# Kernel tuning notes

Measured on AMD Instinct MI355X. Metric: run time of the kernel, lower is better.

Reference implementation:

```python
import jax, jax.numpy as jnp
import numpy as np

B, T, V = 8, 2048, 1024


def setup_inputs() -> dict:
    key = jax.random.key(0)
    k1, k2, k3, k4, k5 = jax.random.split(key, 5)
    idx = jax.random.randint(k1, (B, T), 0, V)
    # nn.Embedding(length, 1) weight, std=0.02
    v = 0.02 * jax.random.normal(k2, (T, 1), dtype=jnp.float32)
    # nn.Linear(V, V, bias=False) weights (torch layout: out x in), std=0.02
    Wk = 0.02 * jax.random.normal(k3, (V, V), dtype=jnp.float32)
    Wq = 0.02 * jax.random.normal(k4, (V, V), dtype=jnp.float32)
    Wv = 0.02 * jax.random.normal(k5, (V, V), dtype=jnp.float32)
    return {"idx": idx, "v": v, "Wk": Wk, "Wq": Wq, "Wv": Wv}


def reference(idx, v, Wk, Wq, Wv):
    Tn = v.shape[0]
    Vn = Wk.shape[0]
    # one-hot token embedding [B, T, V]
    e = jax.nn.one_hot(idx, Vn, dtype=jnp.float32)
    # relative positions, clipped at 0; pos_embd[i, j] = v[i-j] for i >= j else 0
    pos = jnp.arange(Tn)
    rel = jnp.clip(pos[:, None] - pos[None, :], 0)
    pos_embd = jnp.tril(v[rel, 0])  # [T, T]
    # layer_one = pos_embd @ e  -> [B, T, V]
    layer_one = jnp.einsum('ts,bsv->btv', pos_embd, e)
    K = layer_one @ Wk.T           # Linear: x @ W^T
    Q = e @ Wq.T
    attention = jnp.einsum('btv,bsv->bts', Q, K)  # [B, T, T]
    causal = jnp.tril(jnp.ones((Tn, Tn), dtype=bool))
    masked_attention = jnp.where(causal, attention, 0.0)
    output = jnp.einsum('bts,bsv->btv', masked_attention, e @ Wv.T)
    logits = output + 0.001
    return logits
```

## Files before the change

kernel.cpp:

```cpp
#include <hip/hip_runtime.h>
#include <stdint.h>

#define T_DIM 2048
#define V_DIM 1024
#define B_DIM 8
#define NT 16

typedef unsigned int u32;
typedef unsigned short u16;
typedef __attribute__((ext_vector_type(8))) short s16x8;
typedef __attribute__((ext_vector_type(4))) float f32x4;

__device__ __forceinline__ u16 f2bf(float x) {
  u32 u = __builtin_bit_cast(u32, x);
  u = u + 0x7FFFu + ((u >> 16) & 1u);
  return (u16)(u >> 16);
}

#define GLD16(gp, lp) __builtin_amdgcn_global_load_lds( \
    (const __attribute__((address_space(1))) u32*)(gp), \
    (__attribute__((address_space(3))) u32*)(lp), 16, 0, 0)

template<int MODE, bool F32OUT>
__global__ void __launch_bounds__(256, 2)
gemm_bt(const u16* __restrict__ A, int lda, long long batchA,
        const u16* __restrict__ Bt, int ldb, long long batchB,
        void* __restrict__ Cv, int ldc, long long batchC,
        int K, float bias)
{
  int bn, bm, bz;
  if (MODE == 0) {
    bn = blockIdx.x; bm = blockIdx.y; bz = blockIdx.z;
  } else if (MODE == 1) {
    int lam = blockIdx.x;
    int tau = lam >> 3; bz = lam & 7;
    int b = NT - 1, off = 0;
    while (tau >= off + (NT - b)) { off += NT - b; b--; }
    bn = b; bm = b + (tau - off);
  } else {
    int lam = blockIdx.x;
    bm = (NT - 1) - (lam >> 6);
    bn = (lam >> 3) & 7;
    bz = lam & 7;
  }
  const u16* Ab = A + (long long)bz * batchA;
  const u16* Bb = Bt + (long long)bz * batchB;
  int m0 = bm * 128, n0 = bn * 128;
  int kmax = K;
  if (MODE == 1) { int kl = (bn + 1) * 128; kmax = kl < K ? kl : K; }
  if (MODE == 2) { int kl = (bm + 1) * 128; kmax = kl < K ? kl : K; }

  __shared__ u16 As[128 * 64];
  __shared__ u16 Bs[128 * 64];

  int tid = threadIdx.x;
  int lane = tid & 63;
  int wid = tid >> 6;
  int wm = wid >> 1, wn = wid & 1;

  f32x4 acc[4][4] = {};

  int r0 = tid >> 3;
  int gcol = (((tid & 7) - r0) & 7) * 8;
  const u16* ga = Ab + (long long)(m0 + r0) * lda + gcol;
  const u16* gb = Bb + (long long)(n0 + r0) * ldb + gcol;
  u16* la = As + tid * 8;
  u16* lb = Bs + tid * 8;
  long long lda32 = (long long)32 * lda;
  long long ldb32 = (long long)32 * ldb;

  int rm = lane & 15;
  int q = lane >> 4;

  for (int k0 = 0; k0 < kmax; k0 += 64) {
#pragma unroll
    for (int i = 0; i < 4; i++)
      GLD16(ga + k0 + i * lda32, la + i * 2048);
#pragma unroll
    for (int i = 0; i < 4; i++)
      GLD16(gb + k0 + i * ldb32, lb + i * 2048);
    __syncthreads();
#pragma unroll
    for (int ks = 0; ks < 2; ks++) {
      s16x8 af[4], bfv[4];
#pragma unroll
      for (int mi = 0; mi < 4; mi++) {
        int row = wm * 64 + mi * 16 + rm;
        int p = ((ks * 4 + q) + row) & 7;
        af[mi] = *(const s16x8*)&As[row * 64 + p * 8];
      }
#pragma unroll
      for (int ni = 0; ni < 4; ni++) {
        int row = wn * 64 + ni * 16 + rm;
        int p = ((ks * 4 + q) + row) & 7;
        bfv[ni] = *(const s16x8*)&Bs[row * 64 + p * 8];
      }
#pragma unroll
      for (int mi = 0; mi < 4; mi++)
#pragma unroll
        for (int ni = 0; ni < 4; ni++)
          acc[mi][ni] = __builtin_amdgcn_mfma_f32_16x16x32_bf16(
              af[mi], bfv[ni], acc[mi][ni], 0, 0, 0);
    }
    __syncthreads();
  }

  int col = lane & 15;
  int rq = (lane >> 4) * 4;
#pragma unroll
  for (int mi = 0; mi < 4; mi++) {
#pragma unroll
    for (int ni = 0; ni < 4; ni++) {
      int lr = wm * 64 + mi * 16 + rq;
      int lc = wn * 64 + ni * 16 + col;
#pragma unroll
      for (int rr = 0; rr < 4; rr++) {
        float val = acc[mi][ni][rr];
        if (MODE == 1 && (n0 + lc) > (m0 + lr + rr)) val = 0.f;
        long long off = (long long)(m0 + lr + rr) * ldc + (n0 + lc);
        if (F32OUT) {
          float* C = (float*)Cv + (long long)bz * batchC;
          C[off] = val + bias;
        } else {
          u16* C = (u16*)Cv + (long long)bz * batchC;
          C[off] = f2bf(val);
        }
      }
    }
  }
}

#define LDSB 24576
#define FENCE() asm volatile("" ::: "memory")

template<int MODE>
__global__ void __launch_bounds__(512, 2)
gemm8(const u16* __restrict__ Ag, int lda, long long batchA,
      const u16* __restrict__ Btg, int ldb, long long batchB,
      void* __restrict__ Cv, int ldc, long long batchC,
      float bias, int lnb)
{
  int lam = blockIdx.x;
  int bz = lam & ((1 << lnb) - 1);
  int tau = lam >> lnb;
  int m, n;
  if (MODE == 1) {
    int nn = 7, off = 0;
    while (tau >= off + (16 - 2 * nn)) { off += 16 - 2 * nn; nn--; }
    n = nn; m = 2 * nn + (tau - off);
  } else {
    m = 15 - (tau >> 2);
    n = tau & 3;
  }
  const int m0 = m * 128, n0 = n * 256;
  const int nk = (MODE == 1) ? (n + 1) * 4 : (m + 1) * 2;

  const u16* __restrict__ Ab = Ag + (long long)bz * batchA;
  const u16* __restrict__ Bb = Btg + (long long)bz * batchB;

  __shared__ u16 lds[3 * LDSB];

  const int tid = threadIdx.x;
  const int lane = tid & 63;
  const int wid = tid >> 6;
  const int wm = wid >> 2, wn = wid & 3;

  const u16* ga[2]; int la_[2];
#pragma unroll
  for (int i = 0; i < 2; i++) {
    int f = i * 512 + tid, r = f >> 3, c = ((f & 7) - r) & 7;
    ga[i] = Ab + (long long)(m0 + r) * lda + c * 8;
    la_[i] = f * 8;
  }
  const u16* gb[4]; int lb_[4];
#pragma unroll
  for (int i = 0; i < 4; i++) {
    int f = i * 512 + tid, r = f >> 3, c = ((f & 7) - r) & 7;
    gb[i] = Bb + (long long)(n0 + r) * ldb + c * 8;
    lb_[i] = 8192 + f * 8;
  }

  const int rm = lane & 15, q = lane >> 4;
  int aoff[4][2], boff[4][2];
#pragma unroll
  for (int mi = 0; mi < 4; mi++)
#pragma unroll
    for (int ks = 0; ks < 2; ks++) {
      int row = wm * 64 + mi * 16 + rm;
      aoff[mi][ks] = row * 64 + (((ks * 4 + q) + row) & 7) * 8;
    }
#pragma unroll
  for (int ni = 0; ni < 4; ni++)
#pragma unroll
    for (int ks = 0; ks < 2; ks++) {
      int row = wn * 64 + ni * 16 + rm;
      boff[ni][ks] = 8192 + row * 64 + (((ks * 4 + q) + row) & 7) * 8;
    }

  f32x4 acc[4][4] = {};

#pragma unroll
  for (int i = 0; i < 2; i++) GLD16(ga[i], &lds[la_[i]]);
#pragma unroll
  for (int i = 0; i < 4; i++) GLD16(gb[i], &lds[lb_[i]]);
#pragma unroll
  for (int i = 0; i < 2; i++) GLD16(ga[i] + 64, &lds[LDSB + la_[i]]);
#pragma unroll
  for (int i = 0; i < 4; i++) GLD16(gb[i] + 64, &lds[LDSB + lb_[i]]);

  int cb = 0;
  for (int kt = 0; kt < nk; ++kt) {
    if (kt + 1 < nk) asm volatile("s_waitcnt vmcnt(6)" ::: "memory");
    else             asm volatile("s_waitcnt vmcnt(0)" ::: "memory");
    __builtin_amdgcn_s_barrier();
    FENCE();

    const u16* Abuf = &lds[cb];
    int pb = cb + 2 * LDSB; if (pb >= 3 * LDSB) pb -= 3 * LDSB;
    const bool pf = (kt + 2) < nk;
    const int pk = (kt + 2) * 64;

    s16x8 af[4][2], bf0[2][2];
#pragma unroll
    for (int mi = 0; mi < 4; mi++)
#pragma unroll
      for (int ks = 0; ks < 2; ks++)
        af[mi][ks] = *(const s16x8*)&Abuf[aoff[mi][ks]];
#pragma unroll
    for (int ni = 0; ni < 2; ni++)
#pragma unroll
      for (int ks = 0; ks < 2; ks++)
        bf0[ni][ks] = *(const s16x8*)&Abuf[boff[ni][ks]];
    if (pf) {
      GLD16(ga[0] + pk, &lds[pb + la_[0]]);
      GLD16(ga[1] + pk, &lds[pb + la_[1]]);
      GLD16(gb[0] + pk, &lds[pb + lb_[0]]);
    }
    __builtin_amdgcn_s_barrier();
    FENCE();
    __builtin_amdgcn_s_setprio(1);
#pragma unroll
    for (int ks = 0; ks < 2; ks++)
#pragma unroll
      for (int mi = 0; mi < 4; mi++)
#pragma unroll
        for (int ni = 0; ni < 2; ni++)
          acc[mi][ni] = __builtin_amdgcn_mfma_f32_16x16x32_bf16(
              af[mi][ks], bf0[ni][ks], acc[mi][ni], 0, 0, 0);
    __builtin_amdgcn_s_setprio(0);
    __builtin_amdgcn_s_barrier();
    FENCE();

    s16x8 bf1[2][2];
#pragma unroll
    for (int ni = 0; ni < 2; ni++)
#pragma unroll
      for (int ks = 0; ks < 2; ks++)
        bf1[ni][ks] = *(const s16x8*)&Abuf[boff[ni + 2][ks]];
    if (pf) {
      GLD16(gb[1] + pk, &lds[pb + lb_[1]]);
      GLD16(gb[2] + pk, &lds[pb + lb_[2]]);
      GLD16(gb[3] + pk, &lds[pb + lb_[3]]);
    }
    __builtin_amdgcn_s_barrier();
    FENCE();
    __builtin_amdgcn_s_setprio(1);
#pragma unroll
    for (int ks = 0; ks < 2; ks++)
#pragma unroll
      for (int mi = 0; mi < 4; mi++)
#pragma unroll
        for (int ni = 0; ni < 2; ni++)
          acc[mi][ni + 2] = __builtin_amdgcn_mfma_f32_16x16x32_bf16(
              af[mi][ks], bf1[ni][ks], acc[mi][ni + 2], 0, 0, 0);
    __builtin_amdgcn_s_setprio(0);
    cb += LDSB; if (cb >= 3 * LDSB) cb = 0;
  }

  const int col = lane & 15, rq = (lane >> 4) * 4;
  if (MODE == 2) {
    float* C = (float*)Cv + (long long)bz * batchC;
#pragma unroll
    for (int mi = 0; mi < 4; mi++) {
      int lr = m0 + wm * 64 + mi * 16 + rq;
#pragma unroll
      for (int ni = 0; ni < 4; ni++) {
        int lc = n0 + wn * 64 + ni * 16 + col;
#pragma unroll
        for (int rr = 0; rr < 4; rr++)
          C[(long long)(lr + rr) * ldc + lc] = acc[mi][ni][rr] + bias;
      }
    }
  } else {
    u16* C = (u16*)Cv + (long long)bz * batchC;
#pragma unroll
    for (int mi = 0; mi < 4; mi++) {
      int lr = m0 + wm * 64 + mi * 16 + rq;
#pragma unroll
      for (int ni = 0; ni < 4; ni++) {
        int lc = n0 + wn * 64 + ni * 16 + col;
#pragma unroll
        for (int rr = 0; rr < 4; rr++) {
          float val = acc[mi][ni][rr];
          if (lc > lr + rr) val = 0.f;
          C[(long long)(lr + rr) * ldc + lc] = f2bf(val);
        }
      }
    }
  }
}

__global__ void prep_weights(const float* __restrict__ Wq, u16* __restrict__ WqT,
                             const float* __restrict__ Wk, u16* __restrict__ WkT,
                             const float* __restrict__ Wv, u16* __restrict__ Wvb)
{
  int z = blockIdx.z;
  if (z == 2) {
    int bx = blockIdx.y * 32 + blockIdx.x;
    int i = bx * 1024 + threadIdx.y * 32 + threadIdx.x;
#pragma unroll
    for (int k = 0; k < 4; k++) Wvb[i + k * 256] = f2bf(Wv[i + k * 256]);
    return;
  }
  const float* src = z ? Wk : Wq;
  u16* dst = z ? WkT : WqT;
  __shared__ float tile[32][33];
  int x0 = blockIdx.x * 32, y0 = blockIdx.y * 32;
  int tx = threadIdx.x, ty = threadIdx.y;
#pragma unroll
  for (int k = 0; k < 4; k++)
    tile[ty + k * 8][tx] = src[(long long)(y0 + ty + k * 8) * V_DIM + x0 + tx];
  __syncthreads();
#pragma unroll
  for (int k = 0; k < 4; k++)
    dst[(long long)(x0 + ty + k * 8) * V_DIM + y0 + tx] = f2bf(tile[tx][ty + k * 8]);
}

__global__ void build_p(const float* __restrict__ v, u16* __restrict__ P)
{
  int gid = blockIdx.x * 256 + threadIdx.x;
  int e0 = gid * 8;
  int s = e0 >> 11, u0 = e0 & 2047;
  s16x8 o;
#pragma unroll
  for (int k = 0; k < 8; k++) {
    int u = u0 + k;
    o[k] = (short)((u <= s) ? f2bf(v[s - u]) : (u16)0);
  }
  *(s16x8*)&P[e0] = o;
}

__global__ void __launch_bounds__(256)
gather_gy(const int* __restrict__ idx, const u16* __restrict__ Mb,
          const u16* __restrict__ Wvb, u16* __restrict__ G,
          u16* __restrict__ Yt, int b0)
{
  int bx = blockIdx.x, z = blockIdx.y;
  const int* idxrow = idx + (long long)(b0 + z) * T_DIM;
  __shared__ u16 Row[V_DIM];
  int tid = threadIdx.x;
  const u32* src;
  u16* dst;
  if (bx < T_DIM) {
    src = (const u32*)(Mb + (long long)idxrow[bx] * V_DIM);
    dst = G + ((long long)z * T_DIM + bx) * T_DIM;
  } else {
    src = (const u32*)(Wvb + (long long)(bx - T_DIM) * V_DIM);
    dst = Yt + ((long long)z * V_DIM + (bx - T_DIM)) * T_DIM;
  }
  u32* dstl = (u32*)Row;
  dstl[tid] = src[tid];
  dstl[tid + 256] = src[tid + 256];
  __syncthreads();
  int s0 = tid * 8;
  int4 i0 = *(const int4*)&idxrow[s0];
  int4 i1 = *(const int4*)&idxrow[s0 + 4];
  s16x8 o;
  o[0] = (short)Row[i0.x]; o[1] = (short)Row[i0.y];
  o[2] = (short)Row[i0.z]; o[3] = (short)Row[i0.w];
  o[4] = (short)Row[i1.x]; o[5] = (short)Row[i1.y];
  o[6] = (short)Row[i1.z]; o[7] = (short)Row[i1.w];
  *(s16x8*)&dst[s0] = o;
}

extern "C" void kernel_launch(void* const* d_in, const int* in_sizes, int n_in,
                              void* d_out, int out_size, void* d_ws, size_t ws_size,
                              hipStream_t stream)
{
  const int*   idx = (const int*)d_in[0];
  const float* v   = (const float*)d_in[1];
  const float* Wk  = (const float*)d_in[2];
  const float* Wq  = (const float*)d_in[3];
  const float* Wv  = (const float*)d_in[4];
  float* out = (float*)d_out;

  char* p = (char*)d_ws;
  const size_t SZ_VV = (size_t)V_DIM * V_DIM * 2;
  const size_t SZ_TT = (size_t)T_DIM * T_DIM * 2;
  const size_t SZ_VT = (size_t)V_DIM * T_DIM * 2;
  u16* WqT = (u16*)p; p += SZ_VV;
  u16* WkT = (u16*)p; p += SZ_VV;
  u16* Wvb = (u16*)p; p += SZ_VV;
  u16* Mb  = (u16*)p; p += SZ_VV;
  u16* P   = (u16*)p; p += SZ_TT;
  size_t used = (size_t)(p - (char*)d_ws);
  size_t per = 2 * SZ_TT + SZ_VT;
  int nb = 8;
  while (nb > 1 && used + (size_t)nb * per > ws_size) nb >>= 1;
  u16* G    = (u16*)p; p += (size_t)nb * SZ_TT;
  u16* Abuf = (u16*)p; p += (size_t)nb * SZ_TT;
  u16* Yt   = (u16*)p;
  int lnb = (nb == 8) ? 3 : (nb == 4) ? 2 : (nb == 2) ? 1 : 0;

  prep_weights<<<dim3(32, 32, 3), dim3(32, 8), 0, stream>>>(Wq, WqT, Wk, WkT, Wv, Wvb);
  build_p<<<2048, 256, 0, stream>>>(v, P);
  gemm_bt<0, false><<<dim3(V_DIM / 128, V_DIM / 128, 1), 256, 0, stream>>>(
      WqT, V_DIM, 0, WkT, V_DIM, 0, Mb, V_DIM, 0, V_DIM, 0.f);

  for (int b0 = 0; b0 < B_DIM; b0 += nb) {
    gather_gy<<<dim3(T_DIM + V_DIM, nb), 256, 0, stream>>>(idx, Mb, Wvb, G, Yt, b0);
    gemm8<1><<<dim3(72 * nb), 512, 0, stream>>>(
        G, T_DIM, (long long)T_DIM * T_DIM, P, T_DIM, 0,
        Abuf, T_DIM, (long long)T_DIM * T_DIM, 0.f, lnb);
    gemm8<2><<<dim3(64 * nb), 512, 0, stream>>>(
        Abuf, T_DIM, (long long)T_DIM * T_DIM, Yt, T_DIM, (long long)V_DIM * T_DIM,
        out + (long long)b0 * T_DIM * V_DIM, V_DIM, (long long)T_DIM * V_DIM,
        0.001f, lnb);
  }
}
```

Before: 203.9 us.

## Enlarge gemm8 tiles to 256x256 with double-buffered LDS and four-phase pipeline

The causal/triangular GEMM kernels move from 128x256 output tiles with a triple-buffered LDS ring to 256x256 tiles with two LDS buffers. Each wave now owns an 8x4 grid of MFMA accumulators, and the K-step is split into four MFMA phases with global-to-LDS prefetches interleaved between them. The goal is to raise arithmetic intensity and cut global and LDS traffic per FLOP. In exchange, accumulator register pressure doubles, the grid halves to fewer workgroups, and triangular work is handled at coarser granularity. The unused triangular modes of gemm_bt are also removed.

```diff
diff --git a/kernel.cpp b/kernel.cpp
--- a/kernel.cpp
+++ b/kernel.cpp
@@ -28,27 +28,11 @@
         void* __restrict__ Cv, int ldc, long long batchC,
         int K, float bias)
 {
-  int bn, bm, bz;
-  if (MODE == 0) {
-    bn = blockIdx.x; bm = blockIdx.y; bz = blockIdx.z;
-  } else if (MODE == 1) {
-    int lam = blockIdx.x;
-    int tau = lam >> 3; bz = lam & 7;
-    int b = NT - 1, off = 0;
-    while (tau >= off + (NT - b)) { off += NT - b; b--; }
-    bn = b; bm = b + (tau - off);
-  } else {
-    int lam = blockIdx.x;
-    bm = (NT - 1) - (lam >> 6);
-    bn = (lam >> 3) & 7;
-    bz = lam & 7;
-  }
+  int bn = blockIdx.x, bm = blockIdx.y, bz = blockIdx.z;
   const u16* Ab = A + (long long)bz * batchA;
   const u16* Bb = Bt + (long long)bz * batchB;
   int m0 = bm * 128, n0 = bn * 128;
   int kmax = K;
-  if (MODE == 1) { int kl = (bn + 1) * 128; kmax = kl < K ? kl : K; }
-  if (MODE == 2) { int kl = (bm + 1) * 128; kmax = kl < K ? kl : K; }
 
   __shared__ u16 As[128 * 64];
   __shared__ u16 Bs[128 * 64];
@@ -116,7 +100,6 @@
 #pragma unroll
       for (int rr = 0; rr < 4; rr++) {
         float val = acc[mi][ni][rr];
-        if (MODE == 1 && (n0 + lc) > (m0 + lr + rr)) val = 0.f;
         long long off = (long long)(m0 + lr + rr) * ldc + (n0 + lc);
         if (F32OUT) {
           float* C = (float*)Cv + (long long)bz * batchC;
@@ -130,7 +113,7 @@
   }
 }
 
-#define LDSB 24576
+#define LDSE 32768
 #define FENCE() asm volatile("" ::: "memory")
 
 template<int MODE>
@@ -146,98 +129,79 @@
   int m, n;
   if (MODE == 1) {
     int nn = 7, off = 0;
-    while (tau >= off + (16 - 2 * nn)) { off += 16 - 2 * nn; nn--; }
-    n = nn; m = 2 * nn + (tau - off);
+    while (tau >= off + (8 - nn)) { off += 8 - nn; nn--; }
+    n = nn; m = nn + (tau - off);
   } else {
-    m = 15 - (tau >> 2);
+    m = 7 - (tau >> 2);
     n = tau & 3;
   }
-  const int m0 = m * 128, n0 = n * 256;
-  const int nk = (MODE == 1) ? (n + 1) * 4 : (m + 1) * 2;
+  const int m0 = m * 256, n0 = n * 256;
+  const int nk = ((MODE == 1 ? n : m) + 1) * 4;
 
   const u16* __restrict__ Ab = Ag + (long long)bz * batchA;
   const u16* __restrict__ Bb = Btg + (long long)bz * batchB;
 
-  __shared__ u16 lds[3 * LDSB];
+  __shared__ u16 lds[2 * LDSE];
 
   const int tid = threadIdx.x;
   const int lane = tid & 63;
   const int wid = tid >> 6;
   const int wm = wid >> 2, wn = wid & 3;
 
-  const u16* ga[2]; int la_[2];
-#pragma unroll
-  for (int i = 0; i < 2; i++) {
+  const u16* ga[4]; const u16* gb[4]; int la_[4], lb_[4];
+#pragma unroll
+  for (int i = 0; i < 4; i++) {
     int f = i * 512 + tid, r = f >> 3, c = ((f & 7) - r) & 7;
     ga[i] = Ab + (long long)(m0 + r) * lda + c * 8;
+    gb[i] = Bb + (long long)(n0 + r) * ldb + c * 8;
     la_[i] = f * 8;
-  }
-  const u16* gb[4]; int lb_[4];
-#pragma unroll
-  for (int i = 0; i < 4; i++) {
-    int f = i * 512 + tid, r = f >> 3, c = ((f & 7) - r) & 7;
-    gb[i] = Bb + (long long)(n0 + r) * ldb + c * 8;
-    lb_[i] = 8192 + f * 8;
+    lb_[i] = 16384 + f * 8;
   }
 
   const int rm = lane & 15, q = lane >> 4;
-  int aoff[4][2], boff[4][2];
-#pragma unroll
-  for (int mi = 0; mi < 4; mi++)
-#pragma unroll
-    for (int ks = 0; ks < 2; ks++) {
-      int row = wm * 64 + mi * 16 + rm;
-      aoff[mi][ks] = row * 64 + (((ks * 4 + q) + row) & 7) * 8;
-    }
-#pragma unroll
-  for (int ni = 0; ni < 4; ni++)
-#pragma unroll
-    for (int ks = 0; ks < 2; ks++) {
-      int row = wn * 64 + ni * 16 + rm;
-      boff[ni][ks] = 8192 + row * 64 + (((ks * 4 + q) + row) & 7) * 8;
-    }
-
-  f32x4 acc[4][4] = {};
-
-#pragma unroll
-  for (int i = 0; i < 2; i++) GLD16(ga[i], &lds[la_[i]]);
+  const int arow0 = wm * 128 + rm;
+  const int brow0 = wn * 64 + rm;
+  int aoff[2], boff[2];
+#pragma unroll
+  for (int ks = 0; ks < 2; ks++) {
+    aoff[ks] = arow0 * 64 + (((ks * 4 + q) + arow0) & 7) * 8;
+    boff[ks] = 16384 + brow0 * 64 + (((ks * 4 + q) + brow0) & 7) * 8;
+  }
+
+  f32x4 acc[8][4] = {};
+
+#pragma unroll
+  for (int i = 0; i < 4; i++) GLD16(ga[i], &lds[la_[i]]);
 #pragma unroll
   for (int i = 0; i < 4; i++) GLD16(gb[i], &lds[lb_[i]]);
 #pragma unroll
-  for (int i = 0; i < 2; i++) GLD16(ga[i] + 64, &lds[LDSB + la_[i]]);
-#pragma unroll
-  for (int i = 0; i < 4; i++) GLD16(gb[i] + 64, &lds[LDSB + lb_[i]]);
+  for (int i = 0; i < 4; i++) GLD16(ga[i] + 64, &lds[LDSE + la_[i]]);
+#pragma unroll
+  for (int i = 0; i < 4; i++) GLD16(gb[i] + 64, &lds[LDSE + lb_[i]]);
 
   int cb = 0;
   for (int kt = 0; kt < nk; ++kt) {
-    if (kt + 1 < nk) asm volatile("s_waitcnt vmcnt(6)" ::: "memory");
+    if (kt + 1 < nk) asm volatile("s_waitcnt vmcnt(8)" ::: "memory");
     else             asm volatile("s_waitcnt vmcnt(0)" ::: "memory");
     __builtin_amdgcn_s_barrier();
     FENCE();
 
-    const u16* Abuf = &lds[cb];
-    int pb = cb + 2 * LDSB; if (pb >= 3 * LDSB) pb -= 3 * LDSB;
+    const u16* Lb = &lds[cb];
     const bool pf = (kt + 2) < nk;
     const int pk = (kt + 2) * 64;
 
-    s16x8 af[4][2], bf0[2][2];
+    s16x8 af[4][2], b0f[2][2], b1f[2][2];
+
 #pragma unroll
     for (int mi = 0; mi < 4; mi++)
 #pragma unroll
       for (int ks = 0; ks < 2; ks++)
-        af[mi][ks] = *(const s16x8*)&Abuf[aoff[mi][ks]];
+        af[mi][ks] = *(const s16x8*)&Lb[aoff[ks] + mi * 1024];
 #pragma unroll
     for (int ni = 0; ni < 2; ni++)
 #pragma unroll
       for (int ks = 0; ks < 2; ks++)
-        bf0[ni][ks] = *(const s16x8*)&Abuf[boff[ni][ks]];
-    if (pf) {
-      GLD16(ga[0] + pk, &lds[pb + la_[0]]);
-      GLD16(ga[1] + pk, &lds[pb + la_[1]]);
-      GLD16(gb[0] + pk, &lds[pb + lb_[0]]);
-    }
-    __builtin_amdgcn_s_barrier();
-    FENCE();
+        b0f[ni][ks] = *(const s16x8*)&Lb[boff[ks] + ni * 1024];
     __builtin_amdgcn_s_setprio(1);
 #pragma unroll
     for (int ks = 0; ks < 2; ks++)
@@ -246,24 +210,42 @@
 #pragma unroll
         for (int ni = 0; ni < 2; ni++)
           acc[mi][ni] = __builtin_amdgcn_mfma_f32_16x16x32_bf16(
-              af[mi][ks], bf0[ni][ks], acc[mi][ni], 0, 0, 0);
+              af[mi][ks], b0f[ni][ks], acc[mi][ni], 0, 0, 0);
     __builtin_amdgcn_s_setprio(0);
     __builtin_amdgcn_s_barrier();
     FENCE();
 
-    s16x8 bf1[2][2];
 #pragma unroll
     for (int ni = 0; ni < 2; ni++)
 #pragma unroll
       for (int ks = 0; ks < 2; ks++)
-        bf1[ni][ks] = *(const s16x8*)&Abuf[boff[ni + 2][ks]];
+        b1f[ni][ks] = *(const s16x8*)&Lb[boff[ks] + (ni + 2) * 1024];
     if (pf) {
-      GLD16(gb[1] + pk, &lds[pb + lb_[1]]);
-      GLD16(gb[2] + pk, &lds[pb + lb_[2]]);
-      GLD16(gb[3] + pk, &lds[pb + lb_[3]]);
-    }
+      GLD16(ga[0] + pk, &lds[cb + la_[0]]);
+      GLD16(ga[2] + pk, &lds[cb + la_[2]]);
+    }
+    __builtin_amdgcn_s_setprio(1);
+#pragma unroll
+    for (int ks = 0; ks < 2; ks++)
+#pragma unroll
+      for (int mi = 0; mi < 4; mi++)
+#pragma unroll
+        for (int ni = 0; ni < 2; ni++)
+          acc[mi][ni + 2] = __builtin_amdgcn_mfma_f32_16x16x32_bf16(
+              af[mi][ks], b1f[ni][ks], acc[mi][ni + 2], 0, 0, 0);
+    __builtin_amdgcn_s_setprio(0);
     __builtin_amdgcn_s_barrier();
     FENCE();
+
+#pragma unroll
+    for (int mi = 0; mi < 4; mi++)
+#pragma unroll
+      for (int ks = 0; ks < 2; ks++)
+        af[mi][ks] = *(const s16x8*)&Lb[aoff[ks] + (mi + 4) * 1024];
+    if (pf) {
+      GLD16(gb[0] + pk, &lds[cb + lb_[0]]);
+      GLD16(gb[1] + pk, &lds[cb + lb_[1]]);
+    }
     __builtin_amdgcn_s_setprio(1);
 #pragma unroll
     for (int ks = 0; ks < 2; ks++)
@@ -271,18 +253,37 @@
       for (int mi = 0; mi < 4; mi++)
 #pragma unroll
         for (int ni = 0; ni < 2; ni++)
-          acc[mi][ni + 2] = __builtin_amdgcn_mfma_f32_16x16x32_bf16(
-              af[mi][ks], bf1[ni][ks], acc[mi][ni + 2], 0, 0, 0);
+          acc[mi + 4][ni + 2] = __builtin_amdgcn_mfma_f32_16x16x32_bf16(
+              af[mi][ks], b1f[ni][ks], acc[mi + 4][ni + 2], 0, 0, 0);
     __builtin_amdgcn_s_setprio(0);
-    cb += LDSB; if (cb >= 3 * LDSB) cb = 0;
+    __builtin_amdgcn_s_barrier();
+    FENCE();
+
+    if (pf) {
+      GLD16(gb[2] + pk, &lds[cb + lb_[2]]);
+      GLD16(gb[3] + pk, &lds[cb + lb_[3]]);
+      GLD16(ga[1] + pk, &lds[cb + la_[1]]);
+      GLD16(ga[3] + pk, &lds[cb + la_[3]]);
+    }
+    __builtin_amdgcn_s_setprio(1);
+#pragma unroll
+    for (int ks = 0; ks < 2; ks++)
+#pragma unroll
+      for (int mi = 0; mi < 4; mi++)
+#pragma unroll
+        for (int ni = 0; ni < 2; ni++)
+          acc[mi + 4][ni] = __builtin_amdgcn_mfma_f32_16x16x32_bf16(
+              af[mi][ks], b0f[ni][ks], acc[mi + 4][ni], 0, 0, 0);
+    __builtin_amdgcn_s_setprio(0);
+    cb ^= LDSE;
   }
 
   const int col = lane & 15, rq = (lane >> 4) * 4;
   if (MODE == 2) {
     float* C = (float*)Cv + (long long)bz * batchC;
 #pragma unroll
-    for (int mi = 0; mi < 4; mi++) {
-      int lr = m0 + wm * 64 + mi * 16 + rq;
+    for (int mi = 0; mi < 8; mi++) {
+      int lr = m0 + wm * 128 + mi * 16 + rq;
 #pragma unroll
       for (int ni = 0; ni < 4; ni++) {
         int lc = n0 + wn * 64 + ni * 16 + col;
@@ -294,8 +295,8 @@
   } else {
     u16* C = (u16*)Cv + (long long)bz * batchC;
 #pragma unroll
-    for (int mi = 0; mi < 4; mi++) {
-      int lr = m0 + wm * 64 + mi * 16 + rq;
+    for (int mi = 0; mi < 8; mi++) {
+      int lr = m0 + wm * 128 + mi * 16 + rq;
 #pragma unroll
       for (int ni = 0; ni < 4; ni++) {
         int lc = n0 + wn * 64 + ni * 16 + col;
@@ -419,10 +420,10 @@
 
   for (int b0 = 0; b0 < B_DIM; b0 += nb) {
     gather_gy<<<dim3(T_DIM + V_DIM, nb), 256, 0, stream>>>(idx, Mb, Wvb, G, Yt, b0);
-    gemm8<1><<<dim3(72 * nb), 512, 0, stream>>>(
+    gemm8<1><<<dim3(36 * nb), 512, 0, stream>>>(
         G, T_DIM, (long long)T_DIM * T_DIM, P, T_DIM, 0,
         Abuf, T_DIM, (long long)T_DIM * T_DIM, 0.f, lnb);
-    gemm8<2><<<dim3(64 * nb), 512, 0, stream>>>(
+    gemm8<2><<<dim3(32 * nb), 512, 0, stream>>>(
         Abuf, T_DIM, (long long)T_DIM * T_DIM, Yt, T_DIM, (long long)V_DIM * T_DIM,
         out + (long long)b0 * T_DIM * V_DIM, V_DIM, (long long)T_DIM * V_DIM,
         0.001f, lnb);
```

After: 226.2 us. 1.11x slower.
